# Performance work log

Hardware: AMD Instinct MI355X
Metric: run time of the kernel (lower is better)

The kernel has to match this reference:

```python
import jax, jax.numpy as jnp
import numpy as np
import math

N_HEADS = 4


def setup_inputs() -> dict:
    key = jax.random.key(0)
    ks = jax.random.split(key, 5)
    Bs, M, T, C = 4, 190, 512, 64
    x = jax.random.normal(ks[0], (Bs, M, T, C), dtype=jnp.float32)
    s = 1.0 / math.sqrt(C)
    Wq = jax.random.normal(ks[1], (C, C), dtype=jnp.float32) * s
    Wk = jax.random.normal(ks[2], (C, C), dtype=jnp.float32) * s
    Wv = jax.random.normal(ks[3], (C, C), dtype=jnp.float32) * s
    Wp = jax.random.normal(ks[4], (C, C), dtype=jnp.float32) * s
    z = jnp.zeros((C,), dtype=jnp.float32)
    return {"x": x, "Wq": Wq, "bq": z, "Wk": Wk, "bk": z, "Wv": Wv, "bv": z, "Wp": Wp, "bp": z}


def reference(x, Wq, bq, Wk, bk, Wv, bv, Wp, bp):
    # AxialMultiAttention forward, tied=True, linear=False, dropout=0 (eval).
    Bs, M, T, C = x.shape
    N, D = N_HEADS, C // N_HEADS

    def heads(y):  # [Bs,M,T,C] -> [Bs,M,N,T,D]
        return y.reshape(Bs, M, T, N, D).transpose(0, 1, 3, 2, 4)

    q = heads(x @ Wq + bq)
    k = heads(x @ Wk + bk)
    v = heads(x @ Wv + bv)

    # tied: sum queries/keys over the axial (pair) dim M, keepdim -> size-1 axis
    q_t = q.sum(axis=1)  # [Bs,N,T,D]
    k_t = k.sum(axis=1)  # [Bs,N,T,D]
    scale = 1.0 / math.sqrt(D * M)
    weights = jax.nn.softmax(jnp.einsum('bnqd,bnkd->bnqk', q_t, k_t) * scale, axis=-1)  # [Bs,N,T,T]

    # broadcast tied weights across M when multiplying values
    att = jnp.einsum('bnqk,bmnkd->bmnqd', weights, v)  # [Bs,M,N,T,D]
    att = att.transpose(0, 1, 3, 2, 4).reshape(Bs, M, T, N * D)
    out = att @ Wp + bp  # [Bs,M,T,C]

    # a = weights.detach()[0].mean(0): weights has keepdim axis of size 1 in torch,
    # so [0] -> [1,N,T,T] and mean over dim 0 -> [N,T,T]
    a = jax.lax.stop_gradient(weights)[0]  # [N,T,T]
    return out, a
```

## Files before the change

### kernel.cpp

```cpp
#include <hip/hip_runtime.h>

typedef unsigned short ushort_t;
typedef __bf16 bf16x8 __attribute__((ext_vector_type(8)));
typedef float f32x4 __attribute__((ext_vector_type(4)));
typedef float f32x16 __attribute__((ext_vector_type(16)));

#define DEVI __device__ __forceinline__

constexpr int BSZ = 4;
constexpr int MDIM = 190;
constexpr int TDIM = 512;
constexpr int CDIM = 64;

DEVI ushort_t f2bf(float f) {
    union { float f; unsigned int u; } v; v.f = f;
    unsigned int u = v.u;
    u += 0x7FFFu + ((u >> 16) & 1u);
    return (ushort_t)(u >> 16);
}

__global__ __launch_bounds__(256, 4) void k_vproj(const float* __restrict__ x,
                                                  const float* __restrict__ Wv,
                                                  const float* __restrict__ bv,
                                                  ushort_t* __restrict__ vf,
                                                  float* __restrict__ xsp) {
    __shared__ __align__(16) ushort_t xbf[64 * 72];
    __shared__ __align__(16) ushort_t WvT[64 * 72];
    __shared__ __align__(16) ushort_t vst[64 * 72];

    int tid = threadIdx.x;
    int bid = blockIdx.x;
    int mg = bid & 15;
    int tt = (bid >> 4) & 7;
    int b = bid >> 7;
    int t0 = tt * 64;
    int mbase = mg * 12;
    int cnt = (mbase + 12 <= MDIM) ? 12 : (MDIM - mbase);

    int w = tid >> 6, lane = tid & 63;
    int la = lane & 15, lb = lane >> 4;
    int r = tid >> 2, seg = tid & 3;

    int chunk = tid >> 3, u = tid & 7;
    int ksr = chunk >> 3;
    int nn2 = (chunk >> 1) & 3;
    int lhi2 = chunk & 1;
    int d0 = u * 2;

#pragma unroll
    for (int rep = 0; rep < 16; ++rep) {
        int j = rep * 256 + tid;
        int ci = j >> 6, co = j & 63;
        WvT[co * 72 + ci] = f2bf(Wv[j]);
    }
    float bvv[4];
#pragma unroll
    for (int cf = 0; cf < 4; ++cf) bvv[cf] = bv[16 * cf + la];

    float xacc[16];
#pragma unroll
    for (int u2 = 0; u2 < 16; ++u2) xacc[u2] = 0.f;

    const size_t mstride = (size_t)TDIM * CDIM;
    size_t xaddr = ((size_t)(b * MDIM + mbase) * TDIM + t0 + r) * CDIM + seg * 16;

    float4 xv[4];
#pragma unroll
    for (int u2 = 0; u2 < 4; ++u2) xv[u2] = *(const float4*)(x + xaddr + u2 * 4);

    f32x4 zz = {0.f, 0.f, 0.f, 0.f};

    for (int i = 0; i < cnt; ++i) {
#pragma unroll
        for (int u2 = 0; u2 < 4; ++u2) {
            xacc[u2 * 4 + 0] += xv[u2].x;
            xacc[u2 * 4 + 1] += xv[u2].y;
            xacc[u2 * 4 + 2] += xv[u2].z;
            xacc[u2 * 4 + 3] += xv[u2].w;
            ushort4 h;
            h.x = f2bf(xv[u2].x); h.y = f2bf(xv[u2].y);
            h.z = f2bf(xv[u2].z); h.w = f2bf(xv[u2].w);
            *(ushort4*)&xbf[r * 72 + seg * 16 + u2 * 4] = h;
        }
        __syncthreads();

        int inext = (i + 1 < cnt) ? (i + 1) : i;
        size_t xaddr2 = xaddr + (size_t)(inext - i) * mstride;
        float4 xv2[4];
#pragma unroll
        for (int u2 = 0; u2 < 4; ++u2) xv2[u2] = *(const float4*)(x + xaddr2 + u2 * 4);

        f32x4 acc2[4];
#pragma unroll
        for (int cf = 0; cf < 4; ++cf) acc2[cf] = zz;
#pragma unroll
        for (int ks = 0; ks < 2; ++ks) {
            bf16x8 aa = *(const bf16x8*)&xbf[(w * 16 + la) * 72 + ks * 32 + lb * 8];
#pragma unroll
            for (int cf = 0; cf < 4; ++cf) {
                bf16x8 bb = *(const bf16x8*)&WvT[(16 * cf + la) * 72 + ks * 32 + lb * 8];
                acc2[cf] = __builtin_amdgcn_mfma_f32_16x16x32_bf16(aa, bb, acc2[cf], 0, 0, 0);
            }
        }
#pragma unroll
        for (int cf = 0; cf < 4; ++cf) {
            ushort4 h;
            h.x = f2bf(acc2[cf][0] + bvv[cf]);
            h.y = f2bf(acc2[cf][1] + bvv[cf]);
            h.z = f2bf(acc2[cf][2] + bvv[cf]);
            h.w = f2bf(acc2[cf][3] + bvv[cf]);
            *(ushort4*)&vst[(16 * cf + la) * 72 + w * 16 + lb * 4] = h;
        }
        __syncthreads();

        int m = mbase + i;
        int mblk = m >> 2, mrel = m & 3;
        int cg = mrel >> 1, half = mrel & 1;
        size_t vfbase = ((((size_t)(b * 48 + mblk) * 4 + nn2) * 32 + (tt * 4 + ksr)) * 2 + cg) * 512
                      + (size_t)(lhi2 * 32 + half * 16 + d0) * 8;
        uint4 v0 = *(const uint4*)&vst[(nn2 * 16 + d0) * 72 + ksr * 16 + lhi2 * 8];
        uint4 v1 = *(const uint4*)&vst[(nn2 * 16 + d0 + 1) * 72 + ksr * 16 + lhi2 * 8];
        *(uint4*)(vf + vfbase) = v0;
        *(uint4*)(vf + vfbase + 8) = v1;

#pragma unroll
        for (int u2 = 0; u2 < 4; ++u2) xv[u2] = xv2[u2];
        xaddr = xaddr2;
    }

    if (mg == 15) {
        uint4 z4 = {0u, 0u, 0u, 0u};
#pragma unroll
        for (int pm = 190; pm < 192; ++pm) {
            int mblk = pm >> 2, mrel = pm & 3;
            int cg = mrel >> 1, half = mrel & 1;
            size_t vfbase = ((((size_t)(b * 48 + mblk) * 4 + nn2) * 32 + (tt * 4 + ksr)) * 2 + cg) * 512
                          + (size_t)(lhi2 * 32 + half * 16 + d0) * 8;
            *(uint4*)(vf + vfbase) = z4;
            *(uint4*)(vf + vfbase + 8) = z4;
        }
    }

    size_t sbase = ((size_t)(mg * 4 + b) * TDIM + t0 + r) * CDIM + seg * 16;
#pragma unroll
    for (int u2 = 0; u2 < 4; ++u2) {
        float4 o;
        o.x = xacc[u2 * 4 + 0]; o.y = xacc[u2 * 4 + 1];
        o.z = xacc[u2 * 4 + 2]; o.w = xacc[u2 * 4 + 3];
        *(float4*)(xsp + sbase + u2 * 4) = o;
    }
}

__global__ __launch_bounds__(256) void k_xsum2(const float* __restrict__ xsp,
                                               float* __restrict__ xsum) {
    int idx = blockIdx.x * 256 + threadIdx.x;
    float s = 0.f;
#pragma unroll
    for (int p = 0; p < 16; ++p) s += xsp[(size_t)p * 131072 + idx];
    xsum[idx] = s;
}

__global__ __launch_bounds__(256) void k_weights(const float* __restrict__ xsum,
                                                 const float* __restrict__ Wq,
                                                 const float* __restrict__ bq,
                                                 const float* __restrict__ Wk,
                                                 const float* __restrict__ bk,
                                                 ushort_t* __restrict__ wf,
                                                 float* __restrict__ a_out) {
    __shared__ __align__(16) float kt[512][20];
    __shared__ __align__(16) float qt[32][20];
    __shared__ __align__(16) float xs[64][68];
    __shared__ __align__(16) float wcol[64][16];
    __shared__ float kbias[16], qbias[16];
    __shared__ __align__(16) ushort_t rowbuf[32][520];

    int tid = threadIdx.x;
    int bid = blockIdx.x;
    int tcn = bid & 15;
    int n = (bid >> 4) & 3;
    int b = bid >> 6;
    int t0 = tcn * 32;

    for (int j = tid; j < 1024; j += 256) {
        int c = j >> 4, d = j & 15;
        wcol[c][d] = Wk[c * 64 + n * 16 + d];
    }
    if (tid < 16) kbias[tid] = 190.0f * bk[n * 16 + tid];
    if (tid >= 16 && tid < 32) qbias[tid - 16] = 190.0f * bq[n * 16 + tid - 16];
    __syncthreads();

    for (int ch = 0; ch < 8; ++ch) {
        for (int j = tid; j < 4096; j += 256) {
            int t = j >> 6, c = j & 63;
            xs[t][c] = xsum[((size_t)(b * 512) + (ch * 64 + t)) * 64 + c];
        }
        __syncthreads();
#pragma unroll
        for (int o = 0; o < 4; ++o) {
            int oi = o * 256 + tid;
            int t = oi >> 4, d = oi & 15;
            float s = 0.f;
#pragma unroll
            for (int c = 0; c < 64; ++c) s += xs[t][c] * wcol[c][d];
            kt[ch * 64 + t][d] = s + kbias[d];
        }
        __syncthreads();
    }

    for (int j = tid; j < 1024; j += 256) {
        int c = j >> 4, d = j & 15;
        wcol[c][d] = Wq[c * 64 + n * 16 + d];
    }
    for (int j = tid; j < 2048; j += 256) {
        int t = j >> 6, c = j & 63;
        xs[t][c] = xsum[((size_t)(b * 512) + (t0 + t)) * 64 + c];
    }
    __syncthreads();
#pragma unroll
    for (int o = 0; o < 2; ++o) {
        int oi = o * 256 + tid;
        int t = oi >> 4, d = oi & 15;
        float s = 0.f;
#pragma unroll
        for (int c = 0; c < 64; ++c) s += xs[t][c] * wcol[c][d];
        qt[t][d] = s + qbias[d];
    }
    __syncthreads();

    const float scale = 0.01813692f;
    int w = tid >> 6, lane = tid & 63;
    for (int rr = 0; rr < 8; ++rr) {
        int r = w * 8 + rr;
        float qreg[16];
#pragma unroll
        for (int d = 0; d < 16; ++d) qreg[d] = qt[r][d];
        float lv[8];
#pragma unroll
        for (int i = 0; i < 8; ++i) {
            int k = lane + 64 * i;
            const float* kr = &kt[k][0];
            float s = 0.f;
#pragma unroll
            for (int d = 0; d < 16; ++d) s += qreg[d] * kr[d];
            lv[i] = s * scale;
        }
        float mx = lv[0];
#pragma unroll
        for (int i = 1; i < 8; ++i) mx = fmaxf(mx, lv[i]);
#pragma unroll
        for (int off = 32; off >= 1; off >>= 1) mx = fmaxf(mx, __shfl_xor(mx, off));
        float se = 0.f;
#pragma unroll
        for (int i = 0; i < 8; ++i) { lv[i] = __expf(lv[i] - mx); se += lv[i]; }
#pragma unroll
        for (int off = 32; off >= 1; off >>= 1) se += __shfl_xor(se, off);
        float inv = 1.0f / se;

        size_t abase = ((size_t)(n * 512 + (t0 + r))) * 512;
#pragma unroll
        for (int i = 0; i < 8; ++i) {
            float wv = lv[i] * inv;
            rowbuf[r][lane + 64 * i] = f2bf(wv);
            if (b == 0) a_out[abase + lane + 64 * i] = wv;
        }
    }
    __syncthreads();

    size_t wfbase = ((size_t)((b * 4 + n) * 16 + tcn)) * 32 * 512;
#pragma unroll
    for (int p = 0; p < 8; ++p) {
        int id = p * 256 + tid;
        int ks = id >> 6;
        int lf = id & 63;
        int l31 = lf & 31, lhi = lf >> 5;
        uint4 v = *(const uint4*)&rowbuf[l31][ks * 16 + lhi * 8];
        *(uint4*)(wf + wfbase + (size_t)ks * 512 + lf * 8) = v;
    }
}

__global__ __launch_bounds__(256, 2) void k_att(const ushort_t* __restrict__ wf,
                                                const ushort_t* __restrict__ vf,
                                                const float* __restrict__ Wp,
                                                const float* __restrict__ bp,
                                                float* __restrict__ out) {
    __shared__ __align__(16) ushort_t attS[4 * 64 * 68];
    __shared__ __align__(16) ushort_t WpT[64 * 68];

    int tid = threadIdx.x;
    int bid0 = blockIdx.x;
    int bid = (bid0 & 7) * 192 + (bid0 >> 3);
    int ttile = bid & 7;
    int mt = (bid >> 3) % 48;
    int b = bid / 384;

    int w = tid >> 6, lane = tid & 63;
    int l31 = lane & 31, lhi = lane >> 5;
    int n = w;

#pragma unroll
    for (int rep = 0; rep < 16; ++rep) {
        int j = rep * 256 + tid;
        int ci = j >> 6, co = j & 63;
        WpT[co * 68 + ci] = f2bf(Wp[j]);
    }

    unsigned abase[2];
#pragma unroll
    for (int q = 0; q < 2; ++q)
        abase[q] = (unsigned)((((b * 4 + n) * 16 + ttile * 2 + q) * 32) * 512 + lane * 8);
    unsigned bbase[2];
#pragma unroll
    for (int j = 0; j < 2; ++j)
        bbase[j] = (unsigned)(((((b * 48 + mt) * 4 + n) * 32) * 2 + j) * 512 + lane * 8);

    f32x16 acc[2][2];
#pragma unroll
    for (int q = 0; q < 2; ++q)
#pragma unroll
        for (int j = 0; j < 2; ++j) acc[q][j] = (f32x16)(0.f);

    bf16x8 Ae[4][2], Be[4][2], Ao[4][2], Bo[4][2];

#define LOADC(A_, B_, KC) do {                                                    \
    _Pragma("unroll")                                                             \
    for (int kk = 0; kk < 4; ++kk) {                                              \
        int ks = (KC) * 4 + kk;                                                   \
        _Pragma("unroll")                                                         \
        for (int q = 0; q < 2; ++q)                                               \
            A_[kk][q] = *(const bf16x8*)(wf + abase[q] + ks * 512);               \
        _Pragma("unroll")                                                         \
        for (int j = 0; j < 2; ++j)                                               \
            B_[kk][j] = *(const bf16x8*)(vf + bbase[j] + ks * 1024);              \
    }                                                                             \
} while (0)

#define COMPC(A_, B_) do {                                                        \
    _Pragma("unroll")                                                             \
    for (int kk = 0; kk < 4; ++kk)                                                \
        _Pragma("unroll")                                                         \
        for (int q = 0; q < 2; ++q)                                               \
            _Pragma("unroll")                                                     \
            for (int j = 0; j < 2; ++j)                                           \
                acc[q][j] = __builtin_amdgcn_mfma_f32_32x32x16_bf16(A_[kk][q], B_[kk][j], acc[q][j], 0, 0, 0); \
} while (0)

#define VM16 do { asm volatile("s_waitcnt vmcnt(16)" ::: "memory"); __builtin_amdgcn_sched_barrier(0); } while (0)
#define VM0  do { asm volatile("s_waitcnt vmcnt(0)"  ::: "memory"); __builtin_amdgcn_sched_barrier(0); } while (0)

    LOADC(Ae, Be, 0);
    LOADC(Ao, Bo, 1);
#pragma unroll
    for (int kc = 0; kc < 6; kc += 2) {
        VM16;
        COMPC(Ae, Be);
        LOADC(Ae, Be, kc + 2);
        VM16;
        COMPC(Ao, Bo);
        LOADC(Ao, Bo, kc + 3);
    }
    VM16;
    COMPC(Ae, Be);
    VM0;
    COMPC(Ao, Bo);
#undef LOADC
#undef COMPC
#undef VM16
#undef VM0

    float bpv[2];
#pragma unroll
    for (int cf = 0; cf < 2; ++cf) bpv[cf] = bp[cf * 32 + l31];

    __syncthreads();
#pragma unroll
    for (int q = 0; q < 2; ++q)
#pragma unroll
        for (int j = 0; j < 2; ++j) {
            f32x16 a = acc[q][j];
            int mloc = j * 2 + (l31 >> 4);
            int d = l31 & 15;
#pragma unroll
            for (int r = 0; r < 16; ++r) {
                int t = q * 32 + (r & 3) + 8 * (r >> 2) + 4 * lhi;
                attS[(mloc * 64 + t) * 68 + w * 16 + d] = f2bf(a[r]);
            }
        }
    __syncthreads();

    int m = mt * 4 + w;
    size_t obase = ((size_t)(b * 190 + m) * 512 + ttile * 64) * 64;
#pragma unroll
    for (int q = 0; q < 2; ++q) {
        f32x16 acc2[2];
#pragma unroll
        for (int cf = 0; cf < 2; ++cf) acc2[cf] = (f32x16)(0.f);
#pragma unroll
        for (int kk = 0; kk < 4; ++kk) {
            bf16x8 aa = *(const bf16x8*)(attS + (w * 64 + q * 32 + l31) * 68 + kk * 16 + lhi * 8);
#pragma unroll
            for (int cf = 0; cf < 2; ++cf) {
                bf16x8 bbf = *(const bf16x8*)(WpT + (cf * 32 + l31) * 68 + kk * 16 + lhi * 8);
                acc2[cf] = __builtin_amdgcn_mfma_f32_32x32x16_bf16(aa, bbf, acc2[cf], 0, 0, 0);
            }
        }
        if (m < 190) {
#pragma unroll
            for (int cf = 0; cf < 2; ++cf)
#pragma unroll
                for (int r = 0; r < 16; ++r) {
                    int t = q * 32 + (r & 3) + 8 * (r >> 2) + 4 * lhi;
                    int c = cf * 32 + l31;
                    out[obase + (size_t)t * 64 + c] = acc2[cf][r] + bpv[cf];
                }
        }
    }
}

extern "C" void kernel_launch(void* const* d_in, const int* in_sizes, int n_in,
                              void* d_out, int out_size, void* d_ws, size_t ws_size,
                              hipStream_t stream) {
    const float* x  = (const float*)d_in[0];
    const float* Wq = (const float*)d_in[1];
    const float* bq = (const float*)d_in[2];
    const float* Wk = (const float*)d_in[3];
    const float* bk = (const float*)d_in[4];
    const float* Wv = (const float*)d_in[5];
    const float* bv = (const float*)d_in[6];
    const float* Wp = (const float*)d_in[7];
    const float* bp = (const float*)d_in[8];

    float* out = (float*)d_out;
    float* a_out = out + (size_t)BSZ * MDIM * TDIM * CDIM;

    float* xsp = out;

    float* xsum = (float*)d_ws;
    ushort_t* wf = (ushort_t*)((char*)d_ws + 524288);
    ushort_t* vf = (ushort_t*)((char*)d_ws + 524288 + 8388608);

    k_vproj<<<512, 256, 0, stream>>>(x, Wv, bv, vf, xsp);
    k_xsum2<<<512, 256, 0, stream>>>(xsp, xsum);
    k_weights<<<256, 256, 0, stream>>>(xsum, Wq, bq, Wk, bk, wf, a_out);
    k_att<<<1536, 256, 0, stream>>>(wf, vf, Wp, bp, out);
}
```

Measured before the change: 121.2 us.

## Use 512-thread attention blocks sharing weight tiles with a four-stage load pipeline

k_att now runs 8 waves per block, so two m-blocks share one converted Wp tile and the same weight-tile A reads, and the grid is halved. The K loop becomes a four-deep register pipeline of smaller chunks with a workgroup barrier per group, which keeps waves loosely in step so shared A reads can hit cache. The projection epilogue is split into two phases that reuse the same LDS staging buffer, at the cost of extra syncthreads.

```diff
diff --git a/kernel.cpp b/kernel.cpp
--- a/kernel.cpp
+++ b/kernel.cpp
@@ -278,7 +278,7 @@
     }
 }
 
-__global__ __launch_bounds__(256, 2) void k_att(const ushort_t* __restrict__ wf,
+__global__ __launch_bounds__(512, 2) void k_att(const ushort_t* __restrict__ wf,
                                                 const ushort_t* __restrict__ vf,
                                                 const float* __restrict__ Wp,
                                                 const float* __restrict__ bp,
@@ -288,18 +288,20 @@
 
     int tid = threadIdx.x;
     int bid0 = blockIdx.x;
-    int bid = (bid0 & 7) * 192 + (bid0 >> 3);
-    int ttile = bid & 7;
-    int mt = (bid >> 3) % 48;
-    int b = bid / 384;
-
-    int w = tid >> 6, lane = tid & 63;
+    int bid = (bid0 & 7) * 96 + (bid0 >> 3);
+    int tt = bid & 7;
+    int mgrp = (bid >> 3) % 24;
+    int b = bid / 192;
+
+    int wid = tid >> 6, lane = tid & 63;
     int l31 = lane & 31, lhi = lane >> 5;
-    int n = w;
-
-#pragma unroll
-    for (int rep = 0; rep < 16; ++rep) {
-        int j = rep * 256 + tid;
+    int n = wid >> 1;
+    int mh = wid & 1;
+    int mblk = mgrp * 2 + mh;
+
+#pragma unroll
+    for (int rep = 0; rep < 8; ++rep) {
+        int j = rep * 512 + tid;
         int ci = j >> 6, co = j & 63;
         WpT[co * 68 + ci] = f2bf(Wp[j]);
     }
@@ -307,11 +309,11 @@
     unsigned abase[2];
 #pragma unroll
     for (int q = 0; q < 2; ++q)
-        abase[q] = (unsigned)((((b * 4 + n) * 16 + ttile * 2 + q) * 32) * 512 + lane * 8);
+        abase[q] = (unsigned)((((b * 4 + n) * 16 + tt * 2 + q) * 32) * 512 + lane * 8);
     unsigned bbase[2];
 #pragma unroll
     for (int j = 0; j < 2; ++j)
-        bbase[j] = (unsigned)(((((b * 48 + mt) * 4 + n) * 32) * 2 + j) * 512 + lane * 8);
+        bbase[j] = (unsigned)(((((b * 48 + mblk) * 4 + n) * 32) * 2 + j) * 512 + lane * 8);
 
     f32x16 acc[2][2];
 #pragma unroll
@@ -319,12 +321,12 @@
 #pragma unroll
         for (int j = 0; j < 2; ++j) acc[q][j] = (f32x16)(0.f);
 
-    bf16x8 Ae[4][2], Be[4][2], Ao[4][2], Bo[4][2];
-
-#define LOADC(A_, B_, KC) do {                                                    \
+    bf16x8 A0[2][2], B0[2][2], A1[2][2], B1[2][2], A2[2][2], B2[2][2], A3[2][2], B3[2][2];
+
+#define LOADC(A_, B_, PH) do {                                                    \
     _Pragma("unroll")                                                             \
-    for (int kk = 0; kk < 4; ++kk) {                                              \
-        int ks = (KC) * 4 + kk;                                                   \
+    for (int kk = 0; kk < 2; ++kk) {                                              \
+        int ks = (PH) * 2 + kk;                                                   \
         _Pragma("unroll")                                                         \
         for (int q = 0; q < 2; ++q)                                               \
             A_[kk][q] = *(const bf16x8*)(wf + abase[q] + ks * 512);               \
@@ -336,7 +338,7 @@
 
 #define COMPC(A_, B_) do {                                                        \
     _Pragma("unroll")                                                             \
-    for (int kk = 0; kk < 4; ++kk)                                                \
+    for (int kk = 0; kk < 2; ++kk)                                                \
         _Pragma("unroll")                                                         \
         for (int q = 0; q < 2; ++q)                                               \
             _Pragma("unroll")                                                     \
@@ -344,59 +346,65 @@
                 acc[q][j] = __builtin_amdgcn_mfma_f32_32x32x16_bf16(A_[kk][q], B_[kk][j], acc[q][j], 0, 0, 0); \
 } while (0)
 
-#define VM16 do { asm volatile("s_waitcnt vmcnt(16)" ::: "memory"); __builtin_amdgcn_sched_barrier(0); } while (0)
-#define VM0  do { asm volatile("s_waitcnt vmcnt(0)"  ::: "memory"); __builtin_amdgcn_sched_barrier(0); } while (0)
-
-    LOADC(Ae, Be, 0);
-    LOADC(Ao, Bo, 1);
-#pragma unroll
-    for (int kc = 0; kc < 6; kc += 2) {
-        VM16;
-        COMPC(Ae, Be);
-        LOADC(Ae, Be, kc + 2);
-        VM16;
-        COMPC(Ao, Bo);
-        LOADC(Ao, Bo, kc + 3);
-    }
-    VM16;
-    COMPC(Ae, Be);
-    VM0;
-    COMPC(Ao, Bo);
+#define VMW(N) do { asm volatile("s_waitcnt vmcnt(" #N ")" ::: "memory"); __builtin_amdgcn_sched_barrier(0); } while (0)
+
+    LOADC(A0, B0, 0);
+    LOADC(A1, B1, 1);
+    LOADC(A2, B2, 2);
+    LOADC(A3, B3, 3);
+#pragma unroll
+    for (int g = 0; g < 3; ++g) {
+        VMW(24); __builtin_amdgcn_s_barrier();
+        COMPC(A0, B0); LOADC(A0, B0, g * 4 + 4);
+        VMW(24);
+        COMPC(A1, B1); LOADC(A1, B1, g * 4 + 5);
+        VMW(24);
+        COMPC(A2, B2); LOADC(A2, B2, g * 4 + 6);
+        VMW(24);
+        COMPC(A3, B3); LOADC(A3, B3, g * 4 + 7);
+    }
+    VMW(24); COMPC(A0, B0);
+    VMW(16); COMPC(A1, B1);
+    VMW(8);  COMPC(A2, B2);
+    VMW(0);  COMPC(A3, B3);
 #undef LOADC
 #undef COMPC
-#undef VM16
-#undef VM0
+#undef VMW
 
     float bpv[2];
 #pragma unroll
     for (int cf = 0; cf < 2; ++cf) bpv[cf] = bp[cf * 32 + l31];
 
-    __syncthreads();
-#pragma unroll
-    for (int q = 0; q < 2; ++q)
-#pragma unroll
-        for (int j = 0; j < 2; ++j) {
-            f32x16 a = acc[q][j];
-            int mloc = j * 2 + (l31 >> 4);
-            int d = l31 & 15;
-#pragma unroll
-            for (int r = 0; r < 16; ++r) {
-                int t = q * 32 + (r & 3) + 8 * (r >> 2) + 4 * lhi;
-                attS[(mloc * 64 + t) * 68 + w * 16 + d] = f2bf(a[r]);
-            }
-        }
-    __syncthreads();
-
-    int m = mt * 4 + w;
-    size_t obase = ((size_t)(b * 190 + m) * 512 + ttile * 64) * 64;
-#pragma unroll
-    for (int q = 0; q < 2; ++q) {
+    int mrel2 = wid >> 1;
+    int th = wid & 1;
+
+#pragma unroll
+    for (int h = 0; h < 2; ++h) {
+        __syncthreads();
+        if (mh == h) {
+#pragma unroll
+            for (int q = 0; q < 2; ++q)
+#pragma unroll
+                for (int j = 0; j < 2; ++j) {
+                    f32x16 a = acc[q][j];
+                    int mloc = j * 2 + (l31 >> 4);
+                    int d = l31 & 15;
+#pragma unroll
+                    for (int r = 0; r < 16; ++r) {
+                        int t = q * 32 + (r & 3) + 8 * (r >> 2) + 4 * lhi;
+                        attS[(mloc * 64 + t) * 68 + n * 16 + d] = f2bf(a[r]);
+                    }
+                }
+        }
+        __syncthreads();
+
+        int m = mgrp * 8 + h * 4 + mrel2;
         f32x16 acc2[2];
 #pragma unroll
         for (int cf = 0; cf < 2; ++cf) acc2[cf] = (f32x16)(0.f);
 #pragma unroll
         for (int kk = 0; kk < 4; ++kk) {
-            bf16x8 aa = *(const bf16x8*)(attS + (w * 64 + q * 32 + l31) * 68 + kk * 16 + lhi * 8);
+            bf16x8 aa = *(const bf16x8*)(attS + (mrel2 * 64 + th * 32 + l31) * 68 + kk * 16 + lhi * 8);
 #pragma unroll
             for (int cf = 0; cf < 2; ++cf) {
                 bf16x8 bbf = *(const bf16x8*)(WpT + (cf * 32 + l31) * 68 + kk * 16 + lhi * 8);
@@ -404,11 +412,12 @@
             }
         }
         if (m < 190) {
+            size_t obase = ((size_t)(b * 190 + m) * 512 + tt * 64) * 64;
 #pragma unroll
             for (int cf = 0; cf < 2; ++cf)
 #pragma unroll
                 for (int r = 0; r < 16; ++r) {
-                    int t = q * 32 + (r & 3) + 8 * (r >> 2) + 4 * lhi;
+                    int t = th * 32 + (r & 3) + 8 * (r >> 2) + 4 * lhi;
                     int c = cf * 32 + l31;
                     out[obase + (size_t)t * 64 + c] = acc2[cf][r] + bpv[cf];
                 }
@@ -441,5 +450,5 @@
     k_vproj<<<512, 256, 0, stream>>>(x, Wv, bv, vf, xsp);
     k_xsum2<<<512, 256, 0, stream>>>(xsp, xsum);
     k_weights<<<256, 256, 0, stream>>>(xsum, Wq, bq, Wk, bk, wf, a_out);
-    k_att<<<1536, 256, 0, stream>>>(wf, vf, Wp, bp, out);
-}
+    k_att<<<768, 512, 0, stream>>>(wf, vf, Wp, bp, out);
+}
```

Result: slower. 124.4 us (+2.7%).

## Double k_att T-tile per block and switch to triple-buffered K-step loads

Applied to the files above, without the earlier changes.

Each k_att block now covers 128 query rows (4 A fragments) instead of 64, so every V fragment is reused across twice as many MFMAs, and the grid shrinks from 1536 to 768 blocks. The K loop is restructured into per-K-step loads with three rotating register buffers and vmcnt waits. The epilogue then handles two 64-row halves in turn through the same shared tile. The aim is less V traffic per unit of compute and fewer blocks, at the cost of more accumulator registers (possible occupancy drop) and less parallelism.

```diff
diff --git a/kernel.cpp b/kernel.cpp
--- a/kernel.cpp
+++ b/kernel.cpp
@@ -288,10 +288,11 @@
 
     int tid = threadIdx.x;
     int bid0 = blockIdx.x;
-    int bid = (bid0 & 7) * 192 + (bid0 >> 3);
-    int ttile = bid & 7;
-    int mt = (bid >> 3) % 48;
-    int b = bid / 384;
+    int bid = (bid0 & 7) * 96 + (bid0 >> 3);
+    int mgrp = bid % 48;
+    int panel = bid / 48;
+    int tt = panel & 3;
+    int b = panel >> 2;
 
     int w = tid >> 6, lane = tid & 63;
     int l31 = lane & 31, lhi = lane >> 5;
@@ -304,114 +305,109 @@
         WpT[co * 68 + ci] = f2bf(Wp[j]);
     }
 
-    unsigned abase[2];
-#pragma unroll
-    for (int q = 0; q < 2; ++q)
-        abase[q] = (unsigned)((((b * 4 + n) * 16 + ttile * 2 + q) * 32) * 512 + lane * 8);
+    unsigned abase[4];
+#pragma unroll
+    for (int q = 0; q < 4; ++q)
+        abase[q] = (unsigned)((((b * 4 + n) * 16 + tt * 4 + q) * 32) * 512 + lane * 8);
     unsigned bbase[2];
 #pragma unroll
     for (int j = 0; j < 2; ++j)
-        bbase[j] = (unsigned)(((((b * 48 + mt) * 4 + n) * 32) * 2 + j) * 512 + lane * 8);
-
-    f32x16 acc[2][2];
-#pragma unroll
-    for (int q = 0; q < 2; ++q)
+        bbase[j] = (unsigned)(((((b * 48 + mgrp) * 4 + n) * 32) * 2 + j) * 512 + lane * 8);
+
+    f32x16 acc[4][2];
+#pragma unroll
+    for (int q = 0; q < 4; ++q)
 #pragma unroll
         for (int j = 0; j < 2; ++j) acc[q][j] = (f32x16)(0.f);
 
-    bf16x8 Ae[4][2], Be[4][2], Ao[4][2], Bo[4][2];
-
-#define LOADC(A_, B_, KC) do {                                                    \
+    bf16x8 A0[4], B0[2], A1[4], B1[2], A2[4], B2[2];
+
+#define LOADC(A_, B_, KS) do {                                                    \
     _Pragma("unroll")                                                             \
-    for (int kk = 0; kk < 4; ++kk) {                                              \
-        int ks = (KC) * 4 + kk;                                                   \
-        _Pragma("unroll")                                                         \
-        for (int q = 0; q < 2; ++q)                                               \
-            A_[kk][q] = *(const bf16x8*)(wf + abase[q] + ks * 512);               \
+    for (int q = 0; q < 4; ++q)                                                   \
+        A_[q] = *(const bf16x8*)(wf + abase[q] + (KS) * 512);                     \
+    _Pragma("unroll")                                                             \
+    for (int j = 0; j < 2; ++j)                                                   \
+        B_[j] = *(const bf16x8*)(vf + bbase[j] + (KS) * 1024);                    \
+} while (0)
+
+#define COMPC(A_, B_) do {                                                        \
+    _Pragma("unroll")                                                             \
+    for (int q = 0; q < 4; ++q)                                                   \
         _Pragma("unroll")                                                         \
         for (int j = 0; j < 2; ++j)                                               \
-            B_[kk][j] = *(const bf16x8*)(vf + bbase[j] + ks * 1024);              \
-    }                                                                             \
+            acc[q][j] = __builtin_amdgcn_mfma_f32_32x32x16_bf16(A_[q], B_[j], acc[q][j], 0, 0, 0); \
 } while (0)
 
-#define COMPC(A_, B_) do {                                                        \
-    _Pragma("unroll")                                                             \
-    for (int kk = 0; kk < 4; ++kk)                                                \
-        _Pragma("unroll")                                                         \
-        for (int q = 0; q < 2; ++q)                                               \
-            _Pragma("unroll")                                                     \
-            for (int j = 0; j < 2; ++j)                                           \
-                acc[q][j] = __builtin_amdgcn_mfma_f32_32x32x16_bf16(A_[kk][q], B_[kk][j], acc[q][j], 0, 0, 0); \
-} while (0)
-
-#define VM16 do { asm volatile("s_waitcnt vmcnt(16)" ::: "memory"); __builtin_amdgcn_sched_barrier(0); } while (0)
-#define VM0  do { asm volatile("s_waitcnt vmcnt(0)"  ::: "memory"); __builtin_amdgcn_sched_barrier(0); } while (0)
-
-    LOADC(Ae, Be, 0);
-    LOADC(Ao, Bo, 1);
-#pragma unroll
-    for (int kc = 0; kc < 6; kc += 2) {
-        VM16;
-        COMPC(Ae, Be);
-        LOADC(Ae, Be, kc + 2);
-        VM16;
-        COMPC(Ao, Bo);
-        LOADC(Ao, Bo, kc + 3);
-    }
-    VM16;
-    COMPC(Ae, Be);
-    VM0;
-    COMPC(Ao, Bo);
+#define VMW(N) do { asm volatile("s_waitcnt vmcnt(" #N ")" ::: "memory"); __builtin_amdgcn_sched_barrier(0); } while (0)
+
+    LOADC(A0, B0, 0);
+    LOADC(A1, B1, 1);
+    LOADC(A2, B2, 2);
+#pragma unroll
+    for (int g = 0; g < 9; ++g) {
+        VMW(12);  COMPC(A0, B0);  LOADC(A0, B0, g * 3 + 3);
+        VMW(12);  COMPC(A1, B1);  LOADC(A1, B1, g * 3 + 4);
+        VMW(12);  COMPC(A2, B2);  LOADC(A2, B2, g * 3 + 5);
+    }
+    VMW(12);  COMPC(A0, B0);  LOADC(A0, B0, 30);
+    VMW(12);  COMPC(A1, B1);  LOADC(A1, B1, 31);
+    VMW(12);  COMPC(A2, B2);
+    VMW(6);   COMPC(A0, B0);
+    VMW(0);   COMPC(A1, B1);
 #undef LOADC
 #undef COMPC
-#undef VM16
-#undef VM0
+#undef VMW
 
     float bpv[2];
 #pragma unroll
     for (int cf = 0; cf < 2; ++cf) bpv[cf] = bp[cf * 32 + l31];
 
-    __syncthreads();
-#pragma unroll
-    for (int q = 0; q < 2; ++q)
-#pragma unroll
-        for (int j = 0; j < 2; ++j) {
-            f32x16 a = acc[q][j];
-            int mloc = j * 2 + (l31 >> 4);
-            int d = l31 & 15;
-#pragma unroll
-            for (int r = 0; r < 16; ++r) {
-                int t = q * 32 + (r & 3) + 8 * (r >> 2) + 4 * lhi;
-                attS[(mloc * 64 + t) * 68 + w * 16 + d] = f2bf(a[r]);
+    int m = mgrp * 4 + w;
+
+#pragma unroll
+    for (int th = 0; th < 2; ++th) {
+        __syncthreads();
+#pragma unroll
+        for (int qq = 0; qq < 2; ++qq)
+#pragma unroll
+            for (int j = 0; j < 2; ++j) {
+                f32x16 a = acc[th * 2 + qq][j];
+                int mloc = j * 2 + (l31 >> 4);
+                int d = l31 & 15;
+#pragma unroll
+                for (int r = 0; r < 16; ++r) {
+                    int t = qq * 32 + (r & 3) + 8 * (r >> 2) + 4 * lhi;
+                    attS[(mloc * 64 + t) * 68 + n * 16 + d] = f2bf(a[r]);
+                }
             }
-        }
-    __syncthreads();
-
-    int m = mt * 4 + w;
-    size_t obase = ((size_t)(b * 190 + m) * 512 + ttile * 64) * 64;
-#pragma unroll
-    for (int q = 0; q < 2; ++q) {
-        f32x16 acc2[2];
-#pragma unroll
-        for (int cf = 0; cf < 2; ++cf) acc2[cf] = (f32x16)(0.f);
-#pragma unroll
-        for (int kk = 0; kk < 4; ++kk) {
-            bf16x8 aa = *(const bf16x8*)(attS + (w * 64 + q * 32 + l31) * 68 + kk * 16 + lhi * 8);
-#pragma unroll
-            for (int cf = 0; cf < 2; ++cf) {
-                bf16x8 bbf = *(const bf16x8*)(WpT + (cf * 32 + l31) * 68 + kk * 16 + lhi * 8);
-                acc2[cf] = __builtin_amdgcn_mfma_f32_32x32x16_bf16(aa, bbf, acc2[cf], 0, 0, 0);
+        __syncthreads();
+
+        size_t obase = ((size_t)(b * 190 + m) * 512 + tt * 128 + th * 64) * 64;
+#pragma unroll
+        for (int q2 = 0; q2 < 2; ++q2) {
+            f32x16 acc2[2];
+#pragma unroll
+            for (int cf = 0; cf < 2; ++cf) acc2[cf] = (f32x16)(0.f);
+#pragma unroll
+            for (int kk = 0; kk < 4; ++kk) {
+                bf16x8 aa = *(const bf16x8*)(attS + (w * 64 + q2 * 32 + l31) * 68 + kk * 16 + lhi * 8);
+#pragma unroll
+                for (int cf = 0; cf < 2; ++cf) {
+                    bf16x8 bbf = *(const bf16x8*)(WpT + (cf * 32 + l31) * 68 + kk * 16 + lhi * 8);
+                    acc2[cf] = __builtin_amdgcn_mfma_f32_32x32x16_bf16(aa, bbf, acc2[cf], 0, 0, 0);
+                }
             }
-        }
-        if (m < 190) {
-#pragma unroll
-            for (int cf = 0; cf < 2; ++cf)
-#pragma unroll
-                for (int r = 0; r < 16; ++r) {
-                    int t = q * 32 + (r & 3) + 8 * (r >> 2) + 4 * lhi;
-                    int c = cf * 32 + l31;
-                    out[obase + (size_t)t * 64 + c] = acc2[cf][r] + bpv[cf];
-                }
+            if (m < 190) {
+#pragma unroll
+                for (int cf = 0; cf < 2; ++cf)
+#pragma unroll
+                    for (int r = 0; r < 16; ++r) {
+                        int t = q2 * 32 + (r & 3) + 8 * (r >> 2) + 4 * lhi;
+                        int c = cf * 32 + l31;
+                        out[obase + (size_t)t * 64 + c] = acc2[cf][r] + bpv[cf];
+                    }
+            }
         }
     }
 }
@@ -441,5 +437,5 @@
     k_vproj<<<512, 256, 0, stream>>>(x, Wv, bv, vf, xsp);
     k_xsum2<<<512, 256, 0, stream>>>(xsp, xsum);
     k_weights<<<256, 256, 0, stream>>>(xsum, Wq, bq, Wk, bk, wf, a_out);
-    k_att<<<1536, 256, 0, stream>>>(wf, vf, Wp, bp, out);
-}
+    k_att<<<768, 256, 0, stream>>>(wf, vf, Wp, bp, out);
+}
```

New measurement: 123.2 us. About the same (+1.7%).
